# Performance work log

Hardware: AMD Instinct MI355X
Metric: run time of the kernel (lower is better)

## Reference

```python
import jax, jax.numpy as jnp
import numpy as np

N = 65536            # total nodes = B * NODES_PER_GRAPH
E = 524288           # edges (avg degree 8)
B = 64               # graphs per batch
NODES_PER_GRAPH = 1024
KS = 3               # SplineConv kernel_size per pseudo-dim
DEG = 2              # B-spline degree


def setup_inputs() -> dict:
    key = jax.random.key(0)
    ks = jax.random.split(key, 32)

    def w(k, shape, fan_in):
        return jax.random.normal(k, shape, jnp.float32) * (1.0 / np.sqrt(fan_in))

    inp = {
        "x": jax.random.normal(ks[0], (N, 16), jnp.float32),
        "edge_index": jax.random.randint(ks[1], (2, E), 0, N, jnp.int64),
        "pos": jax.random.uniform(ks[2], (E, 2), jnp.float32),  # pseudo-coords in [0,1]
        "batch": jnp.sort(jax.random.randint(ks[3], (N,), 0, B, jnp.int64)),
    }
    dims = [("enc0", 16, 32), ("enc1", 32, 64), ("enc2", 64, 64),
            ("dec0", 128, 64), ("dec1", 96, 32)]
    for i, (name, ci, co) in enumerate(dims):
        inp[name + "_W"] = w(ks[4 + 3 * i], (KS * KS, ci, co), ci * KS * KS)
        inp[name + "_root"] = w(ks[5 + 3 * i], (ci, co), ci)
        inp[name + "_b"] = jnp.zeros((co,), jnp.float32)
    inp["lin1_W"] = w(ks[20], (NODES_PER_GRAPH * 32, 128), NODES_PER_GRAPH * 32)
    inp["lin1_b"] = jnp.zeros((128,), jnp.float32)
    inp["lin2_W"] = w(ks[21], (128, 3), 128)
    inp["lin2_b"] = jnp.zeros((3,), jnp.float32)
    return inp


def _spline_basis(pseudo):
    """Open B-spline basis, degree 2, kernel_size 3, dim 2 (torch_spline_conv math).
    Returns basis [E, 9] and flattened weight indices [E, 9]."""
    v = pseudo * (KS - DEG)                    # scale to [0, ks-deg] = [0, 1]
    f = v - jnp.floor(v)                       # fractional part [E, 2]
    base = jnp.floor(v).astype(jnp.int32)
    # quadratic B-spline pieces for offsets s = 0, 1, 2
    b = jnp.stack([0.5 * (1.0 - f) ** 2, -f * f + f + 0.5, 0.5 * f * f], axis=-1)  # [E,2,3]
    idx = jnp.clip(base[..., None] + jnp.arange(3), 0, KS - 1)                      # [E,2,3]
    basis = (b[:, 0, :, None] * b[:, 1, None, :]).reshape(-1, 9)                    # [E,9]
    widx = (idx[:, 0, :, None] + KS * idx[:, 1, None, :]).reshape(-1, 9)            # [E,9]
    return basis, widx


def _spline_conv(x, src, dst, basis, widx, W, root, bias, n):
    """SplineConv: per-node transform under each of K kernels, then edge-wise
    basis-weighted gather, mean-scatter to targets, plus root linear + bias."""
    xW = jnp.einsum('ni,kio->nko', x, W)       # [N, 9, out]
    msg = basis[:, 0:1] * xW[src, widx[:, 0]]
    for s in range(1, 9):                      # fixed S = (deg+1)^2 = 9 taps
        msg = msg + basis[:, s:s + 1] * xW[src, widx[:, s]]
    agg = jax.ops.segment_sum(msg, dst, num_segments=n)
    deg = jax.ops.segment_sum(jnp.ones((msg.shape[0],), msg.dtype), dst, num_segments=n)
    out = agg / jnp.maximum(deg, 1.0)[:, None]  # mean aggregation (PyG default)
    return out + x @ root + bias


def _relu6(x):
    return jnp.clip(x, 0.0, 6.0)


def reference(x, edge_index, pos, batch,
              enc0_W, enc0_root, enc0_b,
              enc1_W, enc1_root, enc1_b,
              enc2_W, enc2_root, enc2_b,
              dec0_W, dec0_root, dec0_b,
              dec1_W, dec1_root, dec1_b,
              lin1_W, lin1_b, lin2_W, lin2_b):
    src, dst = edge_index[0], edge_index[1]
    basis, widx = _spline_basis(pos)
    n = x.shape[0]
    outs = [x]
    for W, R, bb in [(enc0_W, enc0_root, enc0_b),
                     (enc1_W, enc1_root, enc1_b),
                     (enc2_W, enc2_root, enc2_b)]:
        outs.append(_relu6(_spline_conv(outs[-1], src, dst, basis, widx, W, R, bb, n)))
    # decoder with skip-concat (encoder_bn/decoder_bn are never used in forward)
    d_in = jnp.concatenate([outs[3], outs[2]], axis=1)                 # 64+64 = 128
    dout = _relu6(_spline_conv(d_in, src, dst, basis, widx, dec0_W, dec0_root, dec0_b, n))
    d_in = jnp.concatenate([dout, outs[1]], axis=1)                    # 64+32 = 96
    dout = _relu6(_spline_conv(d_in, src, dst, basis, widx, dec1_W, dec1_root, dec1_b, n))
    flat = dout.reshape(B, NODES_PER_GRAPH * 32)                       # batch_size = max(batch)+1 = 64 (static)
    h = jax.nn.relu(flat @ lin1_W + lin1_b)
    return h @ lin2_W + lin2_b
```

## Files before the change

kernel.cpp:

```cpp
#include <hip/hip_runtime.h>

#define KS 3
#define NN 65536
#define EE 524288
#define BB 64

typedef unsigned short u16;
typedef unsigned int u32;

typedef __attribute__((ext_vector_type(8))) short bf16x8;
typedef __attribute__((ext_vector_type(4))) float f32x4;

__device__ __forceinline__ float bf2f(u16 u) {
  union { u32 i; float f; } v; v.i = ((u32)u) << 16; return v.f;
}
__device__ __forceinline__ u16 f2bf(float f) {
  union { float f; u32 i; } v; v.f = f;
  u32 x = v.i;
  x += 0x7fffu + ((x >> 16) & 1u);
  return (u16)(x >> 16);
}

static const size_t O_CR   = 0;
static const size_t O_ROWS = 10485760;
static const size_t O_CURS = 10748160;
static const size_t O_BSUM = 11010304;
static const size_t O_BMAT = 11011328;
static const size_t O_XB   = 11379968;
static const size_t O_H1   = 13477184;
static const size_t O_H2   = 17671488;
static const size_t O_H3   = 26060096;
static const size_t O_D0   = 34448704;
static const size_t O_D1   = 42837312;
static const size_t O_HBUF = 47031616;
static const size_t O_DEG  = 47064384;

__global__ void cvt_x(const float* __restrict__ x, u16* __restrict__ xb) {
  int i = blockIdx.x * 256 + threadIdx.x;
  xb[i] = f2bf(x[i]);
}

__global__ void hist_kernel(const int* __restrict__ ei, int* __restrict__ deg) {
  int e = blockIdx.x * 256 + threadIdx.x;
  int d = ei[EE + e]; d = min(max(d, 0), NN - 1);
  atomicAdd(&deg[d], 1);
}

__global__ void scan1(const int* __restrict__ deg, int* __restrict__ rows,
                      int* __restrict__ bsum) {
  __shared__ int s[256];
  int t = threadIdx.x, b = blockIdx.x, i = b * 256 + t;
  int v = deg[i];
  s[t] = v; __syncthreads();
  for (int off = 1; off < 256; off <<= 1) {
    int x = (t >= off) ? s[t - off] : 0; __syncthreads();
    s[t] += x; __syncthreads();
  }
  rows[i] = s[t] - v;
  if (t == 255) bsum[b] = s[255];
}
__global__ void scan2(int* __restrict__ bsum) {
  __shared__ int s[256];
  int t = threadIdx.x;
  int v = bsum[t];
  s[t] = v; __syncthreads();
  for (int off = 1; off < 256; off <<= 1) {
    int x = (t >= off) ? s[t - off] : 0; __syncthreads();
    s[t] += x; __syncthreads();
  }
  bsum[t] = s[t] - v;
}
__global__ void scan3(int* __restrict__ rows, const int* __restrict__ bsum,
                      int* __restrict__ cursor) {
  int t = threadIdx.x, b = blockIdx.x, i = b * 256 + t;
  int v = rows[i] + bsum[b];
  rows[i] = v;
  cursor[i] = v;
  if (i == NN - 1) rows[NN] = EE;
}

__global__ void fill_kernel(const int* __restrict__ ei, const float* __restrict__ pos,
                            int* __restrict__ cursor, u32* __restrict__ cr) {
  int e = blockIdx.x * 256 + threadIdx.x;
  int src = ei[e];      src = min(max(src, 0), NN - 1);
  int dst = ei[EE + e]; dst = min(max(dst, 0), NN - 1);
  float2 p = ((const float2*)pos)[e];
  float fl0 = floorf(p.x), fl1 = floorf(p.y);
  float f0 = p.x - fl0, f1 = p.y - fl1;
  int b0 = (int)fl0, b1 = (int)fl1;
  float w0[3] = { 0.5f*(1.f-f0)*(1.f-f0), -f0*f0+f0+0.5f, 0.5f*f0*f0 };
  float w1[3] = { 0.5f*(1.f-f1)*(1.f-f1), -f1*f1+f1+0.5f, 0.5f*f1*f1 };
  int i0[3], i1[3];
#pragma unroll
  for (int s = 0; s < 3; ++s) {
    i0[s] = min(max(b0 + s, 0), KS - 1);
    i1[s] = min(max(b1 + s, 0), KS - 1);
  }
  float c[9] = {0,0,0,0,0,0,0,0,0};
#pragma unroll
  for (int s0 = 0; s0 < 3; ++s0)
#pragma unroll
    for (int s1 = 0; s1 < 3; ++s1)
      c[i0[s0] + KS * i1[s1]] += w0[s0] * w1[s1];
  u16 h[9];
#pragma unroll
  for (int k = 0; k < 9; ++k) h[k] = f2bf(c[k]);
  int slot = atomicAdd(&cursor[dst], 1);
  slot = min(max(slot, 0), EE - 1);
  size_t b = (size_t)slot * 5;
  cr[b + 0] = (u32)(u16)src | ((u32)h[0] << 16);
  cr[b + 1] = (u32)h[1] | ((u32)h[2] << 16);
  cr[b + 2] = (u32)h[3] | ((u32)h[4] << 16);
  cr[b + 3] = (u32)h[5] | ((u32)h[6] << 16);
  cr[b + 4] = (u32)h[7] | ((u32)h[8] << 16);
}

struct BDesc { const float* W; int dstOff, i0, INW, OUT, K, isRoot; };
struct BDescs { BDesc d[18]; };

__global__ void build_b(BDescs ds, u16* __restrict__ bmat) {
  BDesc d = ds.d[blockIdx.y];
  int idx = blockIdx.x * 256 + threadIdx.x;
  int elems = d.K * d.OUT;
  if (idx >= elems) return;
  int o = idx / d.K, r = idx - o * d.K;
  float v;
  if (d.isRoot) {
    v = (r < d.INW) ? d.W[(size_t)(d.i0 + r) * d.OUT + o] : 0.f;
  } else {
    int kk = r >> 5, ii = r & 31;
    int i = d.i0 + ii;
    v = (i < d.INW) ? d.W[((size_t)kk * d.INW + i) * d.OUT + o] : 0.f;
  }
  bmat[(size_t)d.dstOff + (size_t)o * d.K + r] = f2bf(v);
}

struct PD { const u16* src; int IN, mode, nc, bOff; };
struct RD { const u16* src; int astride, ksteps, bOff; };
struct FArgs { PD ch[2]; RD rt[2]; int nch, nrt; const float* bias; u16* dst; };

#define NSTRIDE 600

template <int OUT>
__global__ __launch_bounds__(256, 8) void fused_layer(FArgs fa, const u32* __restrict__ cr,
                                                      const int* __restrict__ rows,
                                                      const u16* __restrict__ bmat) {
  __shared__ u16 aggl[16 * NSTRIDE];
  constexpr int NT = OUT / 16;
  const int tid = threadIdx.x;
  const int wave = tid >> 6, lane = tid & 63;
  const int quad = lane >> 4, l16 = lane & 15;
  const int l = lane & 31, half = lane >> 5;
  const int nb = blockIdx.x * 16;

  f32x4 C = (f32x4){0.f, 0.f, 0.f, 0.f};

  for (int c = 0; c < fa.nch; ++c) {
    const PD d = fa.ch[c];
    if (d.mode == 0) {
      const u16* sp = d.src + lane;
      const int cslot = (lane >> 5) * 296 + (lane & 31);
      for (int nn = 0; nn < 4; ++nn) {
        const int node = nb + wave * 4 + nn;
        const int rs = rows[node], re = rows[node + 1];
        float a[9] = {0,0,0,0,0,0,0,0,0};
        int r = rs;
        for (; r + 3 < re; r += 4) {
          u32 w0[4]; float xv[4];
#pragma unroll
          for (int g = 0; g < 4; ++g) w0[g] = cr[(size_t)(r + g) * 5];
#pragma unroll
          for (int g = 0; g < 4; ++g)
            xv[g] = bf2f(sp[(size_t)(w0[g] & 0xffffu) * 64]);
#pragma unroll
          for (int g = 0; g < 4; ++g) {
            const u32* p = cr + (size_t)(r + g) * 5;
            u32 q1 = p[1], q2 = p[2], q3 = p[3], q4 = p[4];
            a[0] = fmaf(bf2f((u16)(w0[g] >> 16)), xv[g], a[0]);
            a[1] = fmaf(bf2f((u16)(q1 & 0xffffu)), xv[g], a[1]);
            a[2] = fmaf(bf2f((u16)(q1 >> 16)), xv[g], a[2]);
            a[3] = fmaf(bf2f((u16)(q2 & 0xffffu)), xv[g], a[3]);
            a[4] = fmaf(bf2f((u16)(q2 >> 16)), xv[g], a[4]);
            a[5] = fmaf(bf2f((u16)(q3 & 0xffffu)), xv[g], a[5]);
            a[6] = fmaf(bf2f((u16)(q3 >> 16)), xv[g], a[6]);
            a[7] = fmaf(bf2f((u16)(q4 & 0xffffu)), xv[g], a[7]);
            a[8] = fmaf(bf2f((u16)(q4 >> 16)), xv[g], a[8]);
          }
        }
        for (; r < re; ++r) {
          const u32* p = cr + (size_t)r * 5;
          u32 q0 = p[0];
          float xv = bf2f(sp[(size_t)(q0 & 0xffffu) * 64]);
          u32 q1 = p[1], q2 = p[2], q3 = p[3], q4 = p[4];
          a[0] = fmaf(bf2f((u16)(q0 >> 16)), xv, a[0]);
          a[1] = fmaf(bf2f((u16)(q1 & 0xffffu)), xv, a[1]);
          a[2] = fmaf(bf2f((u16)(q1 >> 16)), xv, a[2]);
          a[3] = fmaf(bf2f((u16)(q2 & 0xffffu)), xv, a[3]);
          a[4] = fmaf(bf2f((u16)(q2 >> 16)), xv, a[4]);
          a[5] = fmaf(bf2f((u16)(q3 & 0xffffu)), xv, a[5]);
          a[6] = fmaf(bf2f((u16)(q3 >> 16)), xv, a[6]);
          a[7] = fmaf(bf2f((u16)(q4 & 0xffffu)), xv, a[7]);
          a[8] = fmaf(bf2f((u16)(q4 >> 16)), xv, a[8]);
        }
        const float inv = 1.f / fmaxf((float)(re - rs), 1.f);
#pragma unroll
        for (int k = 0; k < 9; ++k)
          aggl[(wave * 4 + nn) * NSTRIDE + cslot + k * 32] = f2bf(a[k] * inv);
      }
    } else {
      const int i = l;
      const bool valid = i < d.IN;
      const u16* sp = d.src + i;
      const int IN = d.IN;
      for (int nn = 0; nn < 4; ++nn) {
        const int node = nb + wave * 4 + nn;
        const int rs = rows[node], re = rows[node + 1];
        float a[9] = {0,0,0,0,0,0,0,0,0};
        for (int r = rs + half; r < re; r += 2) {
          const u32* p = cr + (size_t)r * 5;
          u32 q0 = p[0];
          float xv = valid ? bf2f(sp[(size_t)(q0 & 0xffffu) * IN]) : 0.f;
          u32 q1 = p[1], q2 = p[2], q3 = p[3], q4 = p[4];
          a[0] = fmaf(bf2f((u16)(q0 >> 16)), xv, a[0]);
          a[1] = fmaf(bf2f((u16)(q1 & 0xffffu)), xv, a[1]);
          a[2] = fmaf(bf2f((u16)(q1 >> 16)), xv, a[2]);
          a[3] = fmaf(bf2f((u16)(q2 & 0xffffu)), xv, a[3]);
          a[4] = fmaf(bf2f((u16)(q2 >> 16)), xv, a[4]);
          a[5] = fmaf(bf2f((u16)(q3 & 0xffffu)), xv, a[5]);
          a[6] = fmaf(bf2f((u16)(q3 >> 16)), xv, a[6]);
          a[7] = fmaf(bf2f((u16)(q4 & 0xffffu)), xv, a[7]);
          a[8] = fmaf(bf2f((u16)(q4 >> 16)), xv, a[8]);
        }
#pragma unroll
        for (int k = 0; k < 9; ++k) a[k] += __shfl_xor(a[k], 32);
        const float inv = 1.f / fmaxf((float)(re - rs), 1.f);
        if (half == 0) {
#pragma unroll
          for (int k = 0; k < 9; ++k)
            aggl[(wave * 4 + nn) * NSTRIDE + k * 32 + l] = f2bf(a[k] * inv);
        }
      }
    }
    __syncthreads();
    if (wave < NT) {
      for (int cc = 0; cc < d.nc; ++cc) {
        const u16* Bp = bmat + d.bOff + cc * 288 * OUT;
        for (int ks = 0; ks < 9; ++ks) {
          bf16x8 av = *(const bf16x8*)&aggl[l16 * NSTRIDE + cc * 296 + ks * 32 + quad * 8];
          bf16x8 bv = *(const bf16x8*)(Bp + ((size_t)(wave * 16 + l16) * 9 + ks) * 32 + quad * 8);
          C = __builtin_amdgcn_mfma_f32_16x16x32_bf16(av, bv, C, 0, 0, 0);
        }
      }
    }
    __syncthreads();
  }

  if (wave < NT) {
    for (int rx = 0; rx < fa.nrt; ++rx) {
      const RD rd = fa.rt[rx];
      for (int ks = 0; ks < rd.ksteps; ++ks) {
        bf16x8 av = *(const bf16x8*)(rd.src + (size_t)(nb + l16) * rd.astride + ks * 32 + quad * 8);
        bf16x8 bv = *(const bf16x8*)(bmat + rd.bOff
                     + ((size_t)(wave * 16 + l16) * rd.ksteps + ks) * 32 + quad * 8);
        C = __builtin_amdgcn_mfma_f32_16x16x32_bf16(av, bv, C, 0, 0, 0);
      }
    }
#pragma unroll
    for (int r = 0; r < 4; ++r) {
      int node = nb + quad * 4 + r;
      int o = wave * 16 + l16;
      float v = C[r] + fa.bias[o];
      v = fminf(fmaxf(v, 0.f), 6.f);
      fa.dst[(size_t)node * OUT + o] = f2bf(v);
    }
  }
}

__global__ __launch_bounds__(256) void mlp1(const u16* __restrict__ d1,
                                            const float* __restrict__ w1,
                                            float* __restrict__ hbuf) {
  __shared__ __align__(16) u16 bt[128 * 136];
  const int tid = threadIdx.x;
  const int c0 = blockIdx.x * 128;
  for (int idx = tid; idx < 16384; idx += 256) {
    int k = idx >> 7, col = idx & 127;
    bt[col * 136 + k] = f2bf(w1[(size_t)(c0 + k) * 128 + col]);
  }
  __syncthreads();
  const int wave = tid >> 6, lane = tid & 63;
  const int quad = lane >> 4, l16 = lane & 15;
  f32x4 C[8];
#pragma unroll
  for (int nt = 0; nt < 8; ++nt) C[nt] = (f32x4){0.f, 0.f, 0.f, 0.f};
  for (int ks = 0; ks < 4; ++ks) {
    bf16x8 av = *(const bf16x8*)(d1 + (size_t)(wave * 16 + l16) * 32768 + c0 + ks * 32 + quad * 8);
#pragma unroll
    for (int nt = 0; nt < 8; ++nt) {
      bf16x8 bv = *(const bf16x8*)&bt[(nt * 16 + l16) * 136 + ks * 32 + quad * 8];
      C[nt] = __builtin_amdgcn_mfma_f32_16x16x32_bf16(av, bv, C[nt], 0, 0, 0);
    }
  }
#pragma unroll
  for (int nt = 0; nt < 8; ++nt)
#pragma unroll
    for (int r = 0; r < 4; ++r) {
      int g = wave * 16 + quad * 4 + r;
      int o = nt * 16 + l16;
      atomicAdd(&hbuf[g * 128 + o], C[nt][r]);
    }
}

__global__ void mlp2(const float* __restrict__ hbuf, const float* __restrict__ b1,
                     const float* __restrict__ w2, const float* __restrict__ b2,
                     float* __restrict__ out) {
  const int t = threadIdx.x;
  if (t >= BB * 3) return;
  const int g = t / 3, c = t % 3;
  float acc = b2[c];
  for (int j = 0; j < 128; ++j) {
    float h = fmaxf(hbuf[g * 128 + j] + b1[j], 0.f);
    acc = fmaf(h, w2[j * 3 + c], acc);
  }
  out[g * 3 + c] = acc;
}

extern "C" void kernel_launch(void* const* d_in, const int* in_sizes, int n_in,
                              void* d_out, int out_size, void* d_ws, size_t ws_size,
                              hipStream_t stream) {
  const float* x   = (const float*)d_in[0];
  const int*   ei  = (const int*)d_in[1];
  const float* pos = (const float*)d_in[2];

  char* base = (char*)d_ws;
  u32*   cr     = (u32*)(base + O_CR);
  int*   rows   = (int*)(base + O_ROWS);
  int*   cursor = (int*)(base + O_CURS);
  int*   bsum   = (int*)(base + O_BSUM);
  u16*   bmat   = (u16*)(base + O_BMAT);
  u16*   xb     = (u16*)(base + O_XB);
  u16*   h1     = (u16*)(base + O_H1);
  u16*   h2     = (u16*)(base + O_H2);
  u16*   h3     = (u16*)(base + O_H3);
  u16*   d0     = (u16*)(base + O_D0);
  u16*   d1     = (u16*)(base + O_D1);
  float* hbuf   = (float*)(base + O_HBUF);
  int*   deg    = (int*)(base + O_DEG);

  hipMemsetAsync(base + O_HBUF, 0, 32768 + 262144, stream);

  cvt_x<<<NN * 16 / 256, 256, 0, stream>>>(x, xb);
  hist_kernel<<<EE / 256, 256, 0, stream>>>(ei, deg);
  scan1<<<256, 256, 0, stream>>>(deg, rows, bsum);
  scan2<<<1, 256, 0, stream>>>(bsum);
  scan3<<<256, 256, 0, stream>>>(rows, bsum, cursor);
  fill_kernel<<<EE / 256, 256, 0, stream>>>(ei, pos, cursor, cr);

  const float* W_e0 = (const float*)d_in[4];
  const float* R_e0 = (const float*)d_in[5];
  const float* B_e0 = (const float*)d_in[6];
  const float* W_e1 = (const float*)d_in[7];
  const float* R_e1 = (const float*)d_in[8];
  const float* B_e1 = (const float*)d_in[9];
  const float* W_e2 = (const float*)d_in[10];
  const float* R_e2 = (const float*)d_in[11];
  const float* B_e2 = (const float*)d_in[12];
  const float* W_d0 = (const float*)d_in[13];
  const float* R_d0 = (const float*)d_in[14];
  const float* B_d0 = (const float*)d_in[15];
  const float* W_d1 = (const float*)d_in[16];
  const float* R_d1 = (const float*)d_in[17];
  const float* B_d1 = (const float*)d_in[18];

  BDescs ds;
  ds.d[0]  = { W_e0, 0,      0,  16,  32, 288, 0 };
  ds.d[1]  = { W_e1, 9216,   0,  32,  64, 288, 0 };
  ds.d[2]  = { W_e2, 27648,  0,  64,  64, 288, 0 };
  ds.d[3]  = { W_e2, 46080,  32, 64,  64, 288, 0 };
  ds.d[4]  = { W_d0, 64512,  0,  128, 64, 288, 0 };
  ds.d[5]  = { W_d0, 82944,  32, 128, 64, 288, 0 };
  ds.d[6]  = { W_d0, 101376, 64, 128, 64, 288, 0 };
  ds.d[7]  = { W_d0, 119808, 96, 128, 64, 288, 0 };
  ds.d[8]  = { W_d1, 138240, 0,  96,  32, 288, 0 };
  ds.d[9]  = { W_d1, 147456, 32, 96,  32, 288, 0 };
  ds.d[10] = { W_d1, 156672, 64, 96,  32, 288, 0 };
  ds.d[11] = { R_e0, 165888, 0,  16, 32, 32, 1 };
  ds.d[12] = { R_e1, 166912, 0,  32, 64, 32, 1 };
  ds.d[13] = { R_e2, 168960, 0,  64, 64, 64, 1 };
  ds.d[14] = { R_d0, 173056, 0,  64, 64, 64, 1 };
  ds.d[15] = { R_d0, 177152, 64, 64, 64, 64, 1 };
  ds.d[16] = { R_d1, 181248, 0,  64, 32, 64, 1 };
  ds.d[17] = { R_d1, 183296, 64, 32, 32, 32, 1 };
  build_b<<<dim3(72, 18), 256, 0, stream>>>(ds, bmat);

  const int FG = NN / 16;

  FArgs fe0 = { { {xb, 16, 1, 1, 0} }, { {xb, 16, 1, 165888} }, 1, 1, B_e0, h1 };
  fused_layer<32><<<FG, 256, 0, stream>>>(fe0, cr, rows, bmat);

  FArgs fe1 = { { {h1, 32, 1, 1, 9216} }, { {h1, 32, 1, 166912} }, 1, 1, B_e1, h2 };
  fused_layer<64><<<FG, 256, 0, stream>>>(fe1, cr, rows, bmat);

  FArgs fe2 = { { {h2, 64, 0, 2, 27648} }, { {h2, 64, 2, 168960} }, 1, 1, B_e2, h3 };
  fused_layer<64><<<FG, 256, 0, stream>>>(fe2, cr, rows, bmat);

  FArgs fd0 = { { {h3, 64, 0, 2, 64512}, {h2, 64, 0, 2, 101376} },
                { {h3, 64, 2, 173056}, {h2, 64, 2, 177152} }, 2, 2, B_d0, d0 };
  fused_layer<64><<<FG, 256, 0, stream>>>(fd0, cr, rows, bmat);

  FArgs fd1 = { { {d0, 64, 0, 2, 138240}, {h1, 32, 1, 1, 156672} },
                { {d0, 64, 2, 181248}, {h1, 32, 1, 183296} }, 2, 2, B_d1, d1 };
  fused_layer<32><<<FG, 256, 0, stream>>>(fd1, cr, rows, bmat);

  mlp1<<<256, 256, 0, stream>>>(d1, (const float*)d_in[19], hbuf);
  mlp2<<<1, 256, 0, stream>>>(hbuf, (const float*)d_in[20], (const float*)d_in[21],
                              (const float*)d_in[22], (float*)d_out);
}
```

Measured before the change: 689.6 us.

## Reuse enc2 aggregated h2 features in dec0 and deepen gather unrolling

The enc2 layer now writes its per-node aggregated spline features of h2 to a global buffer. dec0 consumes that buffer as a dense 576-wide GEMM operand with a repacked weight block, so it no longer re-gathers h2 over the edges. The edge gather loops are also unrolled further (8-way in mode 0, paired loads in mode 1) to keep more loads in flight. This trades one edge aggregation pass for extra global writes and reads of a 65536x576 bf16 buffer and higher register pressure.

```diff
diff --git a/kernel.cpp b/kernel.cpp
--- a/kernel.cpp
+++ b/kernel.cpp
@@ -34,6 +34,7 @@
 static const size_t O_D1   = 42837312;
 static const size_t O_HBUF = 47031616;
 static const size_t O_DEG  = 47064384;
+static const size_t O_AGG2 = 47326528;
 
 __global__ void cvt_x(const float* __restrict__ x, u16* __restrict__ xb) {
   int i = blockIdx.x * 256 + threadIdx.x;
@@ -115,8 +116,8 @@
   cr[b + 4] = (u32)h[7] | ((u32)h[8] << 16);
 }
 
-struct BDesc { const float* W; int dstOff, i0, INW, OUT, K, isRoot; };
-struct BDescs { BDesc d[18]; };
+struct BDesc { const float* W; int dstOff, i0, INW, OUT, K, type; };
+struct BDescs { BDesc d[17]; };
 
 __global__ void build_b(BDescs ds, u16* __restrict__ bmat) {
   BDesc d = ds.d[blockIdx.y];
@@ -125,8 +126,13 @@
   if (idx >= elems) return;
   int o = idx / d.K, r = idx - o * d.K;
   float v;
-  if (d.isRoot) {
+  if (d.type == 1) {
     v = (r < d.INW) ? d.W[(size_t)(d.i0 + r) * d.OUT + o] : 0.f;
+  } else if (d.type == 2) {
+    int cc = r / 288, rem = r - cc * 288;
+    int kk = rem >> 5, ii = rem & 31;
+    int i = d.i0 + cc * 32 + ii;
+    v = d.W[((size_t)kk * d.INW + i) * d.OUT + o];
   } else {
     int kk = r >> 5, ii = r & 31;
     int i = d.i0 + ii;
@@ -135,11 +141,24 @@
   bmat[(size_t)d.dstOff + (size_t)o * d.K + r] = f2bf(v);
 }
 
-struct PD { const u16* src; int IN, mode, nc, bOff; };
+struct PD { const u16* src; int IN, mode, nc, bOff; u16* aggOut; };
 struct RD { const u16* src; int astride, ksteps, bOff; };
-struct FArgs { PD ch[2]; RD rt[2]; int nch, nrt; const float* bias; u16* dst; };
+struct FArgs { PD ch[2]; RD rt[3]; int nch, nrt; const float* bias; u16* dst; };
 
 #define NSTRIDE 600
+
+#define FW_TAP(W0V, XVV) do {                                   \
+    u32 q1 = p[1], q2 = p[2], q3 = p[3], q4 = p[4];             \
+    a[0] = fmaf(bf2f((u16)((W0V) >> 16)), (XVV), a[0]);         \
+    a[1] = fmaf(bf2f((u16)(q1 & 0xffffu)), (XVV), a[1]);        \
+    a[2] = fmaf(bf2f((u16)(q1 >> 16)), (XVV), a[2]);            \
+    a[3] = fmaf(bf2f((u16)(q2 & 0xffffu)), (XVV), a[3]);        \
+    a[4] = fmaf(bf2f((u16)(q2 >> 16)), (XVV), a[4]);            \
+    a[5] = fmaf(bf2f((u16)(q3 & 0xffffu)), (XVV), a[5]);        \
+    a[6] = fmaf(bf2f((u16)(q3 >> 16)), (XVV), a[6]);            \
+    a[7] = fmaf(bf2f((u16)(q4 & 0xffffu)), (XVV), a[7]);        \
+    a[8] = fmaf(bf2f((u16)(q4 >> 16)), (XVV), a[8]);            \
+  } while (0)
 
 template <int OUT>
 __global__ __launch_bounds__(256, 8) void fused_layer(FArgs fa, const u32* __restrict__ cr,
@@ -159,12 +178,26 @@
     const PD d = fa.ch[c];
     if (d.mode == 0) {
       const u16* sp = d.src + lane;
-      const int cslot = (lane >> 5) * 296 + (lane & 31);
+      const int cslot = half * 296 + l;
+      const int gslot = half * 288 + l;
       for (int nn = 0; nn < 4; ++nn) {
         const int node = nb + wave * 4 + nn;
         const int rs = rows[node], re = rows[node + 1];
         float a[9] = {0,0,0,0,0,0,0,0,0};
         int r = rs;
+        for (; r + 7 < re; r += 8) {
+          u32 w0[8]; float xv[8];
+#pragma unroll
+          for (int g = 0; g < 8; ++g) w0[g] = cr[(size_t)(r + g) * 5];
+#pragma unroll
+          for (int g = 0; g < 8; ++g)
+            xv[g] = bf2f(sp[(size_t)(w0[g] & 0xffffu) * 64]);
+#pragma unroll
+          for (int g = 0; g < 8; ++g) {
+            const u32* p = cr + (size_t)(r + g) * 5;
+            FW_TAP(w0[g], xv[g]);
+          }
+        }
         for (; r + 3 < re; r += 4) {
           u32 w0[4]; float xv[4];
 #pragma unroll
@@ -175,37 +208,29 @@
 #pragma unroll
           for (int g = 0; g < 4; ++g) {
             const u32* p = cr + (size_t)(r + g) * 5;
-            u32 q1 = p[1], q2 = p[2], q3 = p[3], q4 = p[4];
-            a[0] = fmaf(bf2f((u16)(w0[g] >> 16)), xv[g], a[0]);
-            a[1] = fmaf(bf2f((u16)(q1 & 0xffffu)), xv[g], a[1]);
-            a[2] = fmaf(bf2f((u16)(q1 >> 16)), xv[g], a[2]);
-            a[3] = fmaf(bf2f((u16)(q2 & 0xffffu)), xv[g], a[3]);
-            a[4] = fmaf(bf2f((u16)(q2 >> 16)), xv[g], a[4]);
-            a[5] = fmaf(bf2f((u16)(q3 & 0xffffu)), xv[g], a[5]);
-            a[6] = fmaf(bf2f((u16)(q3 >> 16)), xv[g], a[6]);
-            a[7] = fmaf(bf2f((u16)(q4 & 0xffffu)), xv[g], a[7]);
-            a[8] = fmaf(bf2f((u16)(q4 >> 16)), xv[g], a[8]);
+            FW_TAP(w0[g], xv[g]);
           }
         }
         for (; r < re; ++r) {
           const u32* p = cr + (size_t)r * 5;
           u32 q0 = p[0];
           float xv = bf2f(sp[(size_t)(q0 & 0xffffu) * 64]);
-          u32 q1 = p[1], q2 = p[2], q3 = p[3], q4 = p[4];
-          a[0] = fmaf(bf2f((u16)(q0 >> 16)), xv, a[0]);
-          a[1] = fmaf(bf2f((u16)(q1 & 0xffffu)), xv, a[1]);
-          a[2] = fmaf(bf2f((u16)(q1 >> 16)), xv, a[2]);
-          a[3] = fmaf(bf2f((u16)(q2 & 0xffffu)), xv, a[3]);
-          a[4] = fmaf(bf2f((u16)(q2 >> 16)), xv, a[4]);
-          a[5] = fmaf(bf2f((u16)(q3 & 0xffffu)), xv, a[5]);
-          a[6] = fmaf(bf2f((u16)(q3 >> 16)), xv, a[6]);
-          a[7] = fmaf(bf2f((u16)(q4 & 0xffffu)), xv, a[7]);
-          a[8] = fmaf(bf2f((u16)(q4 >> 16)), xv, a[8]);
+          FW_TAP(q0, xv);
         }
         const float inv = 1.f / fmaxf((float)(re - rs), 1.f);
-#pragma unroll
-        for (int k = 0; k < 9; ++k)
-          aggl[(wave * 4 + nn) * NSTRIDE + cslot + k * 32] = f2bf(a[k] * inv);
+        if (d.aggOut) {
+          u16* ao = d.aggOut + (size_t)node * 576 + gslot;
+#pragma unroll
+          for (int k = 0; k < 9; ++k) {
+            u16 v = f2bf(a[k] * inv);
+            aggl[(wave * 4 + nn) * NSTRIDE + cslot + k * 32] = v;
+            ao[k * 32] = v;
+          }
+        } else {
+#pragma unroll
+          for (int k = 0; k < 9; ++k)
+            aggl[(wave * 4 + nn) * NSTRIDE + cslot + k * 32] = f2bf(a[k] * inv);
+        }
       }
     } else {
       const int i = l;
@@ -216,20 +241,25 @@
         const int node = nb + wave * 4 + nn;
         const int rs = rows[node], re = rows[node + 1];
         float a[9] = {0,0,0,0,0,0,0,0,0};
-        for (int r = rs + half; r < re; r += 2) {
+        int r = rs + half;
+        for (; r + 2 < re; r += 4) {
+          u32 w0[2]; float xv[2];
+#pragma unroll
+          for (int g = 0; g < 2; ++g) w0[g] = cr[(size_t)(r + 2 * g) * 5];
+#pragma unroll
+          for (int g = 0; g < 2; ++g)
+            xv[g] = valid ? bf2f(sp[(size_t)(w0[g] & 0xffffu) * IN]) : 0.f;
+#pragma unroll
+          for (int g = 0; g < 2; ++g) {
+            const u32* p = cr + (size_t)(r + 2 * g) * 5;
+            FW_TAP(w0[g], xv[g]);
+          }
+        }
+        for (; r < re; r += 2) {
           const u32* p = cr + (size_t)r * 5;
           u32 q0 = p[0];
           float xv = valid ? bf2f(sp[(size_t)(q0 & 0xffffu) * IN]) : 0.f;
-          u32 q1 = p[1], q2 = p[2], q3 = p[3], q4 = p[4];
-          a[0] = fmaf(bf2f((u16)(q0 >> 16)), xv, a[0]);
-          a[1] = fmaf(bf2f((u16)(q1 & 0xffffu)), xv, a[1]);
-          a[2] = fmaf(bf2f((u16)(q1 >> 16)), xv, a[2]);
-          a[3] = fmaf(bf2f((u16)(q2 & 0xffffu)), xv, a[3]);
-          a[4] = fmaf(bf2f((u16)(q2 >> 16)), xv, a[4]);
-          a[5] = fmaf(bf2f((u16)(q3 & 0xffffu)), xv, a[5]);
-          a[6] = fmaf(bf2f((u16)(q3 >> 16)), xv, a[6]);
-          a[7] = fmaf(bf2f((u16)(q4 & 0xffffu)), xv, a[7]);
-          a[8] = fmaf(bf2f((u16)(q4 >> 16)), xv, a[8]);
+          FW_TAP(q0, xv);
         }
 #pragma unroll
         for (int k = 0; k < 9; ++k) a[k] += __shfl_xor(a[k], 32);
@@ -345,6 +375,7 @@
   u16*   d1     = (u16*)(base + O_D1);
   float* hbuf   = (float*)(base + O_HBUF);
   int*   deg    = (int*)(base + O_DEG);
+  u16*   agg2   = (u16*)(base + O_AGG2);
 
   hipMemsetAsync(base + O_HBUF, 0, 32768 + 262144, stream);
 
@@ -378,36 +409,36 @@
   ds.d[3]  = { W_e2, 46080,  32, 64,  64, 288, 0 };
   ds.d[4]  = { W_d0, 64512,  0,  128, 64, 288, 0 };
   ds.d[5]  = { W_d0, 82944,  32, 128, 64, 288, 0 };
-  ds.d[6]  = { W_d0, 101376, 64, 128, 64, 288, 0 };
-  ds.d[7]  = { W_d0, 119808, 96, 128, 64, 288, 0 };
-  ds.d[8]  = { W_d1, 138240, 0,  96,  32, 288, 0 };
-  ds.d[9]  = { W_d1, 147456, 32, 96,  32, 288, 0 };
-  ds.d[10] = { W_d1, 156672, 64, 96,  32, 288, 0 };
-  ds.d[11] = { R_e0, 165888, 0,  16, 32, 32, 1 };
-  ds.d[12] = { R_e1, 166912, 0,  32, 64, 32, 1 };
-  ds.d[13] = { R_e2, 168960, 0,  64, 64, 64, 1 };
-  ds.d[14] = { R_d0, 173056, 0,  64, 64, 64, 1 };
-  ds.d[15] = { R_d0, 177152, 64, 64, 64, 64, 1 };
-  ds.d[16] = { R_d1, 181248, 0,  64, 32, 64, 1 };
-  ds.d[17] = { R_d1, 183296, 64, 32, 32, 32, 1 };
-  build_b<<<dim3(72, 18), 256, 0, stream>>>(ds, bmat);
+  ds.d[6]  = { W_d0, 101376, 64, 128, 64, 576, 2 };
+  ds.d[7]  = { W_d1, 138240, 0,  96,  32, 288, 0 };
+  ds.d[8]  = { W_d1, 147456, 32, 96,  32, 288, 0 };
+  ds.d[9]  = { W_d1, 156672, 64, 96,  32, 288, 0 };
+  ds.d[10] = { R_e0, 165888, 0,  16, 32, 32, 1 };
+  ds.d[11] = { R_e1, 166912, 0,  32, 64, 32, 1 };
+  ds.d[12] = { R_e2, 168960, 0,  64, 64, 64, 1 };
+  ds.d[13] = { R_d0, 173056, 0,  64, 64, 64, 1 };
+  ds.d[14] = { R_d0, 177152, 64, 64, 64, 64, 1 };
+  ds.d[15] = { R_d1, 181248, 0,  64, 32, 64, 1 };
+  ds.d[16] = { R_d1, 183296, 64, 32, 32, 32, 1 };
+  build_b<<<dim3(144, 17), 256, 0, stream>>>(ds, bmat);
 
   const int FG = NN / 16;
 
-  FArgs fe0 = { { {xb, 16, 1, 1, 0} }, { {xb, 16, 1, 165888} }, 1, 1, B_e0, h1 };
+  FArgs fe0 = { { {xb, 16, 1, 1, 0, nullptr} }, { {xb, 16, 1, 165888} }, 1, 1, B_e0, h1 };
   fused_layer<32><<<FG, 256, 0, stream>>>(fe0, cr, rows, bmat);
 
-  FArgs fe1 = { { {h1, 32, 1, 1, 9216} }, { {h1, 32, 1, 166912} }, 1, 1, B_e1, h2 };
+  FArgs fe1 = { { {h1, 32, 1, 1, 9216, nullptr} }, { {h1, 32, 1, 166912} }, 1, 1, B_e1, h2 };
   fused_layer<64><<<FG, 256, 0, stream>>>(fe1, cr, rows, bmat);
 
-  FArgs fe2 = { { {h2, 64, 0, 2, 27648} }, { {h2, 64, 2, 168960} }, 1, 1, B_e2, h3 };
+  FArgs fe2 = { { {h2, 64, 0, 2, 27648, agg2} }, { {h2, 64, 2, 168960} }, 1, 1, B_e2, h3 };
   fused_layer<64><<<FG, 256, 0, stream>>>(fe2, cr, rows, bmat);
 
-  FArgs fd0 = { { {h3, 64, 0, 2, 64512}, {h2, 64, 0, 2, 101376} },
-                { {h3, 64, 2, 173056}, {h2, 64, 2, 177152} }, 2, 2, B_d0, d0 };
+  FArgs fd0 = { { {h3, 64, 0, 2, 64512, nullptr} },
+                { {agg2, 576, 18, 101376}, {h3, 64, 2, 173056}, {h2, 64, 2, 177152} },
+                1, 3, B_d0, d0 };
   fused_layer<64><<<FG, 256, 0, stream>>>(fd0, cr, rows, bmat);
 
-  FArgs fd1 = { { {d0, 64, 0, 2, 138240}, {h1, 32, 1, 1, 156672} },
+  FArgs fd1 = { { {d0, 64, 0, 2, 138240, nullptr}, {h1, 32, 1, 1, 156672, nullptr} },
                 { {d0, 64, 2, 181248}, {h1, 32, 1, 183296} }, 2, 2, B_d1, d1 };
   fused_layer<32><<<FG, 256, 0, stream>>>(fd1, cr, rows, bmat);
 
```

Result: slower. 712.2 us (+3.3%).

## Fuse decoder skip-concat gathers into one edge pass and halve nodes per block

Applied to the files above, without the earlier changes.

Decoder layers now gather both concatenated inputs (main and skip) in a single pass over each node's edges. This removes the second traversal of the CSR edge/basis records and the extra barrier-separated MFMA phase. Blocks now handle 8 nodes instead of 16 to double the grid, so half of each 16-row MFMA tile is wasted. Edge basis coefficients in the 64-wide path are made wave-uniform via readfirstlane, and the narrow path is unrolled by two edges per half-wave.

```diff
diff --git a/kernel.cpp b/kernel.cpp
--- a/kernel.cpp
+++ b/kernel.cpp
@@ -135,127 +135,170 @@
   bmat[(size_t)d.dstOff + (size_t)o * d.K + r] = f2bf(v);
 }
 
-struct PD { const u16* src; int IN, mode, nc, bOff; };
+struct PD { const u16* src; const u16* src2; int IN, IN2, mode, bOffA, ncA, bOffB, ncB; };
 struct RD { const u16* src; int astride, ksteps, bOff; };
-struct FArgs { PD ch[2]; RD rt[2]; int nch, nrt; const float* bias; u16* dst; };
-
-#define NSTRIDE 600
+struct FArgs { PD ch; RD rt[2]; int nrt; const float* bias; u16* dst; };
+
+#define NSTRIDE 1192
+
+#define DECODE9U(Q0)                                              \
+    u32 q1 = __builtin_amdgcn_readfirstlane(p[1]);                \
+    u32 q2 = __builtin_amdgcn_readfirstlane(p[2]);                \
+    u32 q3 = __builtin_amdgcn_readfirstlane(p[3]);                \
+    u32 q4 = __builtin_amdgcn_readfirstlane(p[4]);                \
+    float c0 = bf2f((u16)((Q0) >> 16));                           \
+    float c1 = bf2f((u16)(q1 & 0xffffu)), c2 = bf2f((u16)(q1 >> 16)); \
+    float c3 = bf2f((u16)(q2 & 0xffffu)), c4 = bf2f((u16)(q2 >> 16)); \
+    float c5 = bf2f((u16)(q3 & 0xffffu)), c6 = bf2f((u16)(q3 >> 16)); \
+    float c7 = bf2f((u16)(q4 & 0xffffu)), c8 = bf2f((u16)(q4 >> 16));
+
+#define DECODE9V(Q0)                                              \
+    u32 q1 = p[1], q2 = p[2], q3 = p[3], q4 = p[4];               \
+    float c0 = bf2f((u16)((Q0) >> 16));                           \
+    float c1 = bf2f((u16)(q1 & 0xffffu)), c2 = bf2f((u16)(q1 >> 16)); \
+    float c3 = bf2f((u16)(q2 & 0xffffu)), c4 = bf2f((u16)(q2 >> 16)); \
+    float c5 = bf2f((u16)(q3 & 0xffffu)), c6 = bf2f((u16)(q3 >> 16)); \
+    float c7 = bf2f((u16)(q4 & 0xffffu)), c8 = bf2f((u16)(q4 >> 16));
+
+#define ACC9(DST, XV) do {                                        \
+    DST[0] = fmaf(c0, (XV), DST[0]); DST[1] = fmaf(c1, (XV), DST[1]); \
+    DST[2] = fmaf(c2, (XV), DST[2]); DST[3] = fmaf(c3, (XV), DST[3]); \
+    DST[4] = fmaf(c4, (XV), DST[4]); DST[5] = fmaf(c5, (XV), DST[5]); \
+    DST[6] = fmaf(c6, (XV), DST[6]); DST[7] = fmaf(c7, (XV), DST[7]); \
+    DST[8] = fmaf(c8, (XV), DST[8]); } while (0)
 
 template <int OUT>
 __global__ __launch_bounds__(256, 8) void fused_layer(FArgs fa, const u32* __restrict__ cr,
                                                       const int* __restrict__ rows,
                                                       const u16* __restrict__ bmat) {
-  __shared__ u16 aggl[16 * NSTRIDE];
+  __shared__ u16 aggl[8 * NSTRIDE];
   constexpr int NT = OUT / 16;
   const int tid = threadIdx.x;
   const int wave = tid >> 6, lane = tid & 63;
   const int quad = lane >> 4, l16 = lane & 15;
   const int l = lane & 31, half = lane >> 5;
-  const int nb = blockIdx.x * 16;
-
-  f32x4 C = (f32x4){0.f, 0.f, 0.f, 0.f};
-
-  for (int c = 0; c < fa.nch; ++c) {
-    const PD d = fa.ch[c];
-    if (d.mode == 0) {
-      const u16* sp = d.src + lane;
-      const int cslot = (lane >> 5) * 296 + (lane & 31);
-      for (int nn = 0; nn < 4; ++nn) {
-        const int node = nb + wave * 4 + nn;
-        const int rs = rows[node], re = rows[node + 1];
-        float a[9] = {0,0,0,0,0,0,0,0,0};
-        int r = rs;
-        for (; r + 3 < re; r += 4) {
-          u32 w0[4]; float xv[4];
-#pragma unroll
-          for (int g = 0; g < 4; ++g) w0[g] = cr[(size_t)(r + g) * 5];
+  const int nb = blockIdx.x * 8;
+
+  const PD d = fa.ch;
+  if (d.mode == 0) {
+    const bool has2 = d.src2 != nullptr;
+    const bool v2 = has2 && (lane < d.IN2);
+    const u16* sp  = d.src + lane;
+    const u16* sp2 = has2 ? d.src2 + (v2 ? lane : 0) : nullptr;
+    const int st2 = d.IN2;
+    const int cslot  = half * 296 + l;
+    const int cslotB = 2 * 296 + half * 296 + l;
+    for (int nn = 0; nn < 2; ++nn) {
+      const int node = nb + wave * 2 + nn;
+      const int rs = rows[node], re = rows[node + 1];
+      float a[9] = {0,0,0,0,0,0,0,0,0};
+      float b9[9] = {0,0,0,0,0,0,0,0,0};
+      int r = rs;
+      for (; r + 3 < re; r += 4) {
+        u32 w0[4]; float xv[4], yv[4];
+#pragma unroll
+        for (int g = 0; g < 4; ++g) w0[g] = cr[(size_t)(r + g) * 5];
+#pragma unroll
+        for (int g = 0; g < 4; ++g)
+          xv[g] = bf2f(sp[(size_t)(w0[g] & 0xffffu) * 64]);
+        if (has2) {
 #pragma unroll
           for (int g = 0; g < 4; ++g)
-            xv[g] = bf2f(sp[(size_t)(w0[g] & 0xffffu) * 64]);
-#pragma unroll
-          for (int g = 0; g < 4; ++g) {
-            const u32* p = cr + (size_t)(r + g) * 5;
-            u32 q1 = p[1], q2 = p[2], q3 = p[3], q4 = p[4];
-            a[0] = fmaf(bf2f((u16)(w0[g] >> 16)), xv[g], a[0]);
-            a[1] = fmaf(bf2f((u16)(q1 & 0xffffu)), xv[g], a[1]);
-            a[2] = fmaf(bf2f((u16)(q1 >> 16)), xv[g], a[2]);
-            a[3] = fmaf(bf2f((u16)(q2 & 0xffffu)), xv[g], a[3]);
-            a[4] = fmaf(bf2f((u16)(q2 >> 16)), xv[g], a[4]);
-            a[5] = fmaf(bf2f((u16)(q3 & 0xffffu)), xv[g], a[5]);
-            a[6] = fmaf(bf2f((u16)(q3 >> 16)), xv[g], a[6]);
-            a[7] = fmaf(bf2f((u16)(q4 & 0xffffu)), xv[g], a[7]);
-            a[8] = fmaf(bf2f((u16)(q4 >> 16)), xv[g], a[8]);
-          }
+            yv[g] = v2 ? bf2f(sp2[(size_t)(w0[g] & 0xffffu) * st2]) : 0.f;
         }
-        for (; r < re; ++r) {
-          const u32* p = cr + (size_t)r * 5;
-          u32 q0 = p[0];
-          float xv = bf2f(sp[(size_t)(q0 & 0xffffu) * 64]);
-          u32 q1 = p[1], q2 = p[2], q3 = p[3], q4 = p[4];
-          a[0] = fmaf(bf2f((u16)(q0 >> 16)), xv, a[0]);
-          a[1] = fmaf(bf2f((u16)(q1 & 0xffffu)), xv, a[1]);
-          a[2] = fmaf(bf2f((u16)(q1 >> 16)), xv, a[2]);
-          a[3] = fmaf(bf2f((u16)(q2 & 0xffffu)), xv, a[3]);
-          a[4] = fmaf(bf2f((u16)(q2 >> 16)), xv, a[4]);
-          a[5] = fmaf(bf2f((u16)(q3 & 0xffffu)), xv, a[5]);
-          a[6] = fmaf(bf2f((u16)(q3 >> 16)), xv, a[6]);
-          a[7] = fmaf(bf2f((u16)(q4 & 0xffffu)), xv, a[7]);
-          a[8] = fmaf(bf2f((u16)(q4 >> 16)), xv, a[8]);
+#pragma unroll
+        for (int g = 0; g < 4; ++g) {
+          const u32* p = cr + (size_t)(r + g) * 5;
+          u32 q0 = __builtin_amdgcn_readfirstlane(w0[g]);
+          DECODE9U(q0);
+          ACC9(a, xv[g]);
+          if (has2) ACC9(b9, yv[g]);
         }
-        const float inv = 1.f / fmaxf((float)(re - rs), 1.f);
+      }
+      for (; r < re; ++r) {
+        const u32* p = cr + (size_t)r * 5;
+        u32 w0 = p[0];
+        float xv = bf2f(sp[(size_t)(w0 & 0xffffu) * 64]);
+        float yv = 0.f;
+        if (has2) yv = v2 ? bf2f(sp2[(size_t)(w0 & 0xffffu) * st2]) : 0.f;
+        u32 q0 = __builtin_amdgcn_readfirstlane(w0);
+        DECODE9U(q0);
+        ACC9(a, xv);
+        if (has2) ACC9(b9, yv);
+      }
+      const float inv = 1.f / fmaxf((float)(re - rs), 1.f);
+      const int row = wave * 2 + nn;
+#pragma unroll
+      for (int k = 0; k < 9; ++k)
+        aggl[row * NSTRIDE + cslot + k * 32] = f2bf(a[k] * inv);
+      if (has2) {
 #pragma unroll
         for (int k = 0; k < 9; ++k)
-          aggl[(wave * 4 + nn) * NSTRIDE + cslot + k * 32] = f2bf(a[k] * inv);
-      }
-    } else {
-      const int i = l;
-      const bool valid = i < d.IN;
-      const u16* sp = d.src + i;
-      const int IN = d.IN;
-      for (int nn = 0; nn < 4; ++nn) {
-        const int node = nb + wave * 4 + nn;
-        const int rs = rows[node], re = rows[node + 1];
-        float a[9] = {0,0,0,0,0,0,0,0,0};
-        for (int r = rs + half; r < re; r += 2) {
-          const u32* p = cr + (size_t)r * 5;
-          u32 q0 = p[0];
-          float xv = valid ? bf2f(sp[(size_t)(q0 & 0xffffu) * IN]) : 0.f;
-          u32 q1 = p[1], q2 = p[2], q3 = p[3], q4 = p[4];
-          a[0] = fmaf(bf2f((u16)(q0 >> 16)), xv, a[0]);
-          a[1] = fmaf(bf2f((u16)(q1 & 0xffffu)), xv, a[1]);
-          a[2] = fmaf(bf2f((u16)(q1 >> 16)), xv, a[2]);
-          a[3] = fmaf(bf2f((u16)(q2 & 0xffffu)), xv, a[3]);
-          a[4] = fmaf(bf2f((u16)(q2 >> 16)), xv, a[4]);
-          a[5] = fmaf(bf2f((u16)(q3 & 0xffffu)), xv, a[5]);
-          a[6] = fmaf(bf2f((u16)(q3 >> 16)), xv, a[6]);
-          a[7] = fmaf(bf2f((u16)(q4 & 0xffffu)), xv, a[7]);
-          a[8] = fmaf(bf2f((u16)(q4 >> 16)), xv, a[8]);
+          aggl[row * NSTRIDE + cslotB + k * 32] = f2bf(b9[k] * inv);
+      }
+    }
+  } else {
+    const int i = l;
+    const bool valid = i < d.IN;
+    const u16* sp = d.src + i;
+    const int IN = d.IN;
+    for (int nn = 0; nn < 2; ++nn) {
+      const int node = nb + wave * 2 + nn;
+      const int rs = rows[node], re = rows[node + 1];
+      float a[9] = {0,0,0,0,0,0,0,0,0};
+      int r = rs + half;
+      for (; r + 2 < re; r += 4) {
+        u32 w0[2]; float xv[2];
+#pragma unroll
+        for (int g = 0; g < 2; ++g) w0[g] = cr[(size_t)(r + 2 * g) * 5];
+#pragma unroll
+        for (int g = 0; g < 2; ++g)
+          xv[g] = valid ? bf2f(sp[(size_t)(w0[g] & 0xffffu) * IN]) : 0.f;
+#pragma unroll
+        for (int g = 0; g < 2; ++g) {
+          const u32* p = cr + (size_t)(r + 2 * g) * 5;
+          u32 q0 = w0[g];
+          DECODE9V(q0);
+          ACC9(a, xv[g]);
         }
-#pragma unroll
-        for (int k = 0; k < 9; ++k) a[k] += __shfl_xor(a[k], 32);
-        const float inv = 1.f / fmaxf((float)(re - rs), 1.f);
-        if (half == 0) {
-#pragma unroll
-          for (int k = 0; k < 9; ++k)
-            aggl[(wave * 4 + nn) * NSTRIDE + k * 32 + l] = f2bf(a[k] * inv);
-        }
-      }
-    }
-    __syncthreads();
-    if (wave < NT) {
-      for (int cc = 0; cc < d.nc; ++cc) {
-        const u16* Bp = bmat + d.bOff + cc * 288 * OUT;
-        for (int ks = 0; ks < 9; ++ks) {
-          bf16x8 av = *(const bf16x8*)&aggl[l16 * NSTRIDE + cc * 296 + ks * 32 + quad * 8];
-          bf16x8 bv = *(const bf16x8*)(Bp + ((size_t)(wave * 16 + l16) * 9 + ks) * 32 + quad * 8);
-          C = __builtin_amdgcn_mfma_f32_16x16x32_bf16(av, bv, C, 0, 0, 0);
-        }
-      }
-    }
-    __syncthreads();
-  }
+      }
+      for (; r < re; r += 2) {
+        const u32* p = cr + (size_t)r * 5;
+        u32 q0 = p[0];
+        float xv = valid ? bf2f(sp[(size_t)(q0 & 0xffffu) * IN]) : 0.f;
+        DECODE9V(q0);
+        ACC9(a, xv);
+      }
+#pragma unroll
+      for (int k = 0; k < 9; ++k) a[k] += __shfl_xor(a[k], 32);
+      const float inv = 1.f / fmaxf((float)(re - rs), 1.f);
+      if (half == 0) {
+#pragma unroll
+        for (int k = 0; k < 9; ++k)
+          aggl[(wave * 2 + nn) * NSTRIDE + k * 32 + l] = f2bf(a[k] * inv);
+      }
+    }
+  }
+  __syncthreads();
 
   if (wave < NT) {
+    f32x4 C = (f32x4){0.f, 0.f, 0.f, 0.f};
+    for (int cc = 0; cc < d.ncA; ++cc) {
+      const u16* Bp = bmat + d.bOffA + cc * 288 * OUT;
+      for (int ks = 0; ks < 9; ++ks) {
+        bf16x8 av = *(const bf16x8*)&aggl[l16 * NSTRIDE + cc * 296 + ks * 32 + quad * 8];
+        bf16x8 bv = *(const bf16x8*)(Bp + ((size_t)(wave * 16 + l16) * 9 + ks) * 32 + quad * 8);
+        C = __builtin_amdgcn_mfma_f32_16x16x32_bf16(av, bv, C, 0, 0, 0);
+      }
+    }
+    for (int cc = 0; cc < d.ncB; ++cc) {
+      const u16* Bp = bmat + d.bOffB + cc * 288 * OUT;
+      for (int ks = 0; ks < 9; ++ks) {
+        bf16x8 av = *(const bf16x8*)&aggl[l16 * NSTRIDE + (2 + cc) * 296 + ks * 32 + quad * 8];
+        bf16x8 bv = *(const bf16x8*)(Bp + ((size_t)(wave * 16 + l16) * 9 + ks) * 32 + quad * 8);
+        C = __builtin_amdgcn_mfma_f32_16x16x32_bf16(av, bv, C, 0, 0, 0);
+      }
+    }
     for (int rx = 0; rx < fa.nrt; ++rx) {
       const RD rd = fa.rt[rx];
       for (int ks = 0; ks < rd.ksteps; ++ks) {
@@ -265,13 +308,15 @@
         C = __builtin_amdgcn_mfma_f32_16x16x32_bf16(av, bv, C, 0, 0, 0);
       }
     }
-#pragma unroll
-    for (int r = 0; r < 4; ++r) {
-      int node = nb + quad * 4 + r;
-      int o = wave * 16 + l16;
-      float v = C[r] + fa.bias[o];
-      v = fminf(fmaxf(v, 0.f), 6.f);
-      fa.dst[(size_t)node * OUT + o] = f2bf(v);
+    if (quad < 2) {
+#pragma unroll
+      for (int r = 0; r < 4; ++r) {
+        int node = nb + quad * 4 + r;
+        int o = wave * 16 + l16;
+        float v = C[r] + fa.bias[o];
+        v = fminf(fmaxf(v, 0.f), 6.f);
+        fa.dst[(size_t)node * OUT + o] = f2bf(v);
+      }
     }
   }
 }
@@ -392,23 +437,26 @@
   ds.d[17] = { R_d1, 183296, 64, 32, 32, 32, 1 };
   build_b<<<dim3(72, 18), 256, 0, stream>>>(ds, bmat);
 
-  const int FG = NN / 16;
-
-  FArgs fe0 = { { {xb, 16, 1, 1, 0} }, { {xb, 16, 1, 165888} }, 1, 1, B_e0, h1 };
+  const int FG = NN / 8;
+
+  FArgs fe0 = { {xb, nullptr, 16, 0, 1, 0, 1, 0, 0},
+                { {xb, 16, 1, 165888}, {} }, 1, B_e0, h1 };
   fused_layer<32><<<FG, 256, 0, stream>>>(fe0, cr, rows, bmat);
 
-  FArgs fe1 = { { {h1, 32, 1, 1, 9216} }, { {h1, 32, 1, 166912} }, 1, 1, B_e1, h2 };
+  FArgs fe1 = { {h1, nullptr, 32, 0, 1, 9216, 1, 0, 0},
+                { {h1, 32, 1, 166912}, {} }, 1, B_e1, h2 };
   fused_layer<64><<<FG, 256, 0, stream>>>(fe1, cr, rows, bmat);
 
-  FArgs fe2 = { { {h2, 64, 0, 2, 27648} }, { {h2, 64, 2, 168960} }, 1, 1, B_e2, h3 };
+  FArgs fe2 = { {h2, nullptr, 64, 0, 0, 27648, 2, 0, 0},
+                { {h2, 64, 2, 168960}, {} }, 1, B_e2, h3 };
   fused_layer<64><<<FG, 256, 0, stream>>>(fe2, cr, rows, bmat);
 
-  FArgs fd0 = { { {h3, 64, 0, 2, 64512}, {h2, 64, 0, 2, 101376} },
-                { {h3, 64, 2, 173056}, {h2, 64, 2, 177152} }, 2, 2, B_d0, d0 };
+  FArgs fd0 = { {h3, h2, 64, 64, 0, 64512, 2, 101376, 2},
+                { {h3, 64, 2, 173056}, {h2, 64, 2, 177152} }, 2, B_d0, d0 };
   fused_layer<64><<<FG, 256, 0, stream>>>(fd0, cr, rows, bmat);
 
-  FArgs fd1 = { { {d0, 64, 0, 2, 138240}, {h1, 32, 1, 1, 156672} },
-                { {d0, 64, 2, 181248}, {h1, 32, 1, 183296} }, 2, 2, B_d1, d1 };
+  FArgs fd1 = { {d0, h1, 64, 32, 0, 138240, 2, 156672, 1},
+                { {d0, 64, 2, 181248}, {h1, 32, 1, 183296} }, 2, B_d1, d1 };
   fused_layer<32><<<FG, 256, 0, stream>>>(fd1, cr, rows, bmat);
 
   mlp1<<<256, 256, 0, stream>>>(d1, (const float*)d_in[19], hbuf);
```

Result: faster. 649.0 us (-5.9%).
